# Performance work log

Measured on AMD Instinct MI355X. Metric: run time of the kernel, lower is better.

The kernel has to match this reference:

```python
import jax, jax.numpy as jnp
import numpy as np

B, S, D, H = 4, 2048, 1024, 16
HD = D // H
SCALE = np.sqrt(HD).astype(np.float32)


def setup_inputs() -> dict:
    key = jax.random.key(0)
    ks = jax.random.split(key, 6)
    std = 1.0 / np.sqrt(D)
    return {
        "query": jax.random.normal(ks[0], (B, S, D), jnp.float32),
        "key": jax.random.normal(ks[1], (B, S, D), jnp.float32),
        "value": jax.random.normal(ks[2], (B, S, D), jnp.float32),
        "Wq": jax.random.normal(ks[3], (D, D), jnp.float32) * std,
        "bq": jnp.zeros((D,), jnp.float32),
        "Wk": jax.random.normal(ks[4], (D, D), jnp.float32) * std,
        "bk": jnp.zeros((D,), jnp.float32),
        "Wv": jax.random.normal(ks[5], (D, D), jnp.float32) * std,
        "bv": jnp.zeros((D,), jnp.float32),
    }


def _split_heads(x):
    # [B,S,D] -> [B,H,S,HD]
    return x.reshape(B, S, H, HD).transpose(0, 2, 1, 3)


def reference(query, key, value, Wq, bq, Wk, bk, Wv, bv):
    q = _split_heads(query @ Wq.T + bq)
    k = _split_heads(key @ Wk.T + bk)
    v = _split_heads(value @ Wv.T + bv)
    scores = jnp.einsum("bhqd,bhkd->bhqk", q, k) / SCALE
    attn = jax.nn.softmax(scores, axis=-1)  # dropout=0 (eval)
    ctx = jnp.einsum("bhqk,bhkd->bhqd", attn, v)
    return ctx.transpose(0, 2, 1, 3).reshape(B, S, D)
```

## Files before the change

### kernel.cpp

```cpp
#include <hip/hip_runtime.h>
#include <hip/hip_bf16.h>

typedef __attribute__((ext_vector_type(8))) short bf16x8;
typedef __attribute__((ext_vector_type(4))) float f32x4;
typedef __attribute__((ext_vector_type(16))) float f32x16;

#define SEQ 2048
#define DMODEL 1024
#define NH 16
#define HD 64
#define BATCH 4
#define BHTOT 64
#define BS 8192
#define QKV_ELEMS 8388608

#define C2EXP 0.1803368801111244f

__device__ __forceinline__ ushort f2bf(float f) {
  union { float f; unsigned u; } v; v.f = f;
  unsigned r = (v.u + 0x7FFFu + ((v.u >> 16) & 1u)) >> 16;
  return (ushort)r;
}

__device__ __forceinline__ unsigned pkbf(float a, float b) {
  union { __hip_bfloat162 h; unsigned u; } cv;
  cv.h = __float22bfloat162_rn(make_float2(a, b));
  return cv.u;
}

#if __has_builtin(__builtin_amdgcn_exp2f)
#define EXP2F(x) __builtin_amdgcn_exp2f(x)
#else
#define EXP2F(x) exp2f(x)
#endif

#define GLD16(gp, lp)                                                        \
  __builtin_amdgcn_global_load_lds(                                          \
      (const __attribute__((address_space(1))) void*)(gp),                   \
      (__attribute__((address_space(3))) void*)(lp), 16, 0, 0)

__global__ __launch_bounds__(256) void convert_w(
    const float* __restrict__ w0, const float* __restrict__ w1,
    const float* __restrict__ w2, ushort* __restrict__ out) {
  const float* src = blockIdx.y == 0 ? w0 : (blockIdx.y == 1 ? w1 : w2);
  size_t e = ((size_t)blockIdx.x * 256 + threadIdx.x) * 4;
  float4 v = *(const float4*)(src + e);
  ushort4 o = { f2bf(v.x), f2bf(v.y), f2bf(v.z), f2bf(v.w) };
  *(ushort4*)(out + (size_t)blockIdx.y * 1048576 + e) = o;
}

__global__ __launch_bounds__(256) void convert_x(
    const float* __restrict__ x0, const float* __restrict__ x1,
    const float* __restrict__ x2, ushort* __restrict__ out) {
  const float* src = blockIdx.y == 0 ? x0 : (blockIdx.y == 1 ? x1 : x2);
  size_t e = ((size_t)blockIdx.x * 256 + threadIdx.x) * 4;
  float4 v = *(const float4*)(src + e);
  ushort4 o = { f2bf(v.x), f2bf(v.y), f2bf(v.z), f2bf(v.w) };
  *(ushort4*)(out + (size_t)blockIdx.y * (size_t)QKV_ELEMS + e) = o;
}

__global__ __launch_bounds__(256) void qkv_gemm_bf(
    const ushort* __restrict__ Xb, const ushort* __restrict__ Wb,
    const float* __restrict__ bq, const float* __restrict__ bk, const float* __restrict__ bv,
    ushort* __restrict__ qkv) {
  __shared__ ushort sA[128][32];
  __shared__ ushort sB[128][32];

  const int z = blockIdx.z;
  const ushort* A = Xb + (size_t)z * QKV_ELEMS;
  const ushort* W = Wb + (size_t)z * 1048576;
  const float* bias = z == 0 ? bq : (z == 1 ? bk : bv);
  const float oscale = z == 0 ? C2EXP : 1.0f;
  ushort* out = qkv + (size_t)z * QKV_ELEMS;

  const int t = threadIdx.x;
  const int m0 = blockIdx.x * 128;
  const int n0 = blockIdx.y * 128;
  const int w = t >> 6, l = t & 63, lr = l & 15, lhi = l >> 4;
  const int wr = (w >> 1) * 64, wc = (w & 1) * 64;

  const int rl = l >> 2;
  const int scol = ((l & 3) * 8) ^ ((rl & 3) << 3);
  const int rcol = (lhi * 8) ^ ((lr & 3) << 3);

  f32x4 acc[4][4];
#pragma unroll
  for (int i = 0; i < 4; i++)
#pragma unroll
    for (int j = 0; j < 4; j++) acc[i][j] = (f32x4){0.f, 0.f, 0.f, 0.f};

  for (int k0 = 0; k0 < DMODEL; k0 += 32) {
#pragma unroll
    for (int i = 0; i < 2; i++) {
      int c = w * 2 + i;
      GLD16(A + (size_t)(m0 + c * 16 + rl) * DMODEL + k0 + scol, &sA[c * 16][0]);
      GLD16(W + (size_t)(n0 + c * 16 + rl) * DMODEL + k0 + scol, &sB[c * 16][0]);
    }
    __syncthreads();
    bf16x8 af[4], bfr[4];
#pragma unroll
    for (int mi = 0; mi < 4; mi++) af[mi] = *(const bf16x8*)(&sA[wr + mi * 16 + lr][rcol]);
#pragma unroll
    for (int ni = 0; ni < 4; ni++) bfr[ni] = *(const bf16x8*)(&sB[wc + ni * 16 + lr][rcol]);
#pragma unroll
    for (int mi = 0; mi < 4; mi++)
#pragma unroll
      for (int ni = 0; ni < 4; ni++)
        acc[mi][ni] = __builtin_amdgcn_mfma_f32_16x16x32_bf16(af[mi], bfr[ni], acc[mi][ni], 0, 0, 0);
    __syncthreads();
  }

#pragma unroll
  for (int mi = 0; mi < 4; mi++) {
#pragma unroll
    for (int ni = 0; ni < 4; ni++) {
      int col = n0 + wc + ni * 16 + lr;
      float bsv = bias[col];
      int h = col >> 6, hd = col & 63;
#pragma unroll
      for (int r = 0; r < 4; r++) {
        int row = m0 + wr + mi * 16 + lhi * 4 + r;
        int b = row >> 11, s = row & 2047;
        float vv = (acc[mi][ni][r] + bsv) * oscale;
        out[(((size_t)(b * NH + h)) * SEQ + s) * HD + hd] = f2bf(vv);
      }
    }
  }
}

__global__ __launch_bounds__(256) void qkv_gemm_f32(
    const float* __restrict__ x0, const float* __restrict__ x1, const float* __restrict__ x2,
    const ushort* __restrict__ Wb,
    const float* __restrict__ bq, const float* __restrict__ bk, const float* __restrict__ bv,
    ushort* __restrict__ qkv) {
  __shared__ ushort sA[128][40];
  __shared__ ushort sB[128][40];

  const int z = blockIdx.z;
  const float* X = z == 0 ? x0 : (z == 1 ? x1 : x2);
  const ushort* W = Wb + (size_t)z * 1048576;
  const float* bias = z == 0 ? bq : (z == 1 ? bk : bv);
  const float oscale = z == 0 ? C2EXP : 1.0f;
  ushort* out = qkv + (size_t)z * QKV_ELEMS;

  const int t = threadIdx.x;
  const int m0 = blockIdx.x * 128;
  const int n0 = blockIdx.y * 128;
  const int w = t >> 6, l = t & 63, lr = l & 15, lhi = l >> 4;
  const int wr = (w >> 1) * 64, wc = (w & 1) * 64;

  f32x4 acc[4][4];
#pragma unroll
  for (int i = 0; i < 4; i++)
#pragma unroll
    for (int j = 0; j < 4; j++) acc[i][j] = (f32x4){0.f, 0.f, 0.f, 0.f};

  for (int k0 = 0; k0 < DMODEL; k0 += 32) {
#pragma unroll
    for (int i = 0; i < 4; i++) {
      int e = i * 256 + t;
      int row = e >> 3, col = (e & 7) * 4;
      float4 a = *(const float4*)(X + (size_t)(m0 + row) * DMODEL + k0 + col);
      ushort4 ab = { f2bf(a.x), f2bf(a.y), f2bf(a.z), f2bf(a.w) };
      *(ushort4*)(&sA[row][col]) = ab;
      ushort4 bb = *(const ushort4*)(W + (size_t)(n0 + row) * DMODEL + k0 + col);
      *(ushort4*)(&sB[row][col]) = bb;
    }
    __syncthreads();
    bf16x8 af[4], bfr[4];
#pragma unroll
    for (int mi = 0; mi < 4; mi++) af[mi] = *(const bf16x8*)(&sA[wr + mi * 16 + lr][lhi * 8]);
#pragma unroll
    for (int ni = 0; ni < 4; ni++) bfr[ni] = *(const bf16x8*)(&sB[wc + ni * 16 + lr][lhi * 8]);
#pragma unroll
    for (int mi = 0; mi < 4; mi++)
#pragma unroll
      for (int ni = 0; ni < 4; ni++)
        acc[mi][ni] = __builtin_amdgcn_mfma_f32_16x16x32_bf16(af[mi], bfr[ni], acc[mi][ni], 0, 0, 0);
    __syncthreads();
  }

#pragma unroll
  for (int mi = 0; mi < 4; mi++) {
#pragma unroll
    for (int ni = 0; ni < 4; ni++) {
      int col = n0 + wc + ni * 16 + lr;
      float bsv = bias[col];
      int h = col >> 6, hd = col & 63;
#pragma unroll
      for (int r = 0; r < 4; r++) {
        int row = m0 + wr + mi * 16 + lhi * 4 + r;
        int b = row >> 11, s = row & 2047;
        float vv = (acc[mi][ni][r] + bsv) * oscale;
        out[(((size_t)(b * NH + h)) * SEQ + s) * HD + hd] = f2bf(vv);
      }
    }
  }
}

__global__ __launch_bounds__(256) void transpose_v(const ushort* __restrict__ vsrc,
                                                   ushort* __restrict__ vtg) {
  __shared__ ushort T[64][72];
  const int s0 = blockIdx.x * 64;
  const int bh = blockIdx.y;
  const int t = threadIdx.x;
  const int r = t >> 2, c16 = (t & 3) * 16;

  const ushort* src = vsrc + ((size_t)bh * SEQ + s0 + r) * HD + c16;
  uint4 a = *(const uint4*)(src);
  uint4 b = *(const uint4*)(src + 8);
  *(uint4*)(&T[r][c16]) = a;
  *(uint4*)(&T[r][c16 + 8]) = b;
  __syncthreads();

  ushort o[16];
#pragma unroll
  for (int jj = 0; jj < 16; jj++) {
    int sj = (jj & 3) | ((jj & 4) << 1) | ((jj & 8) >> 1);
    o[jj] = T[c16 + sj][r];
  }
  ushort* dst = vtg + ((size_t)bh * HD + r) * SEQ + s0 + c16;
  *(uint4*)(dst) = *(uint4*)(&o[0]);
  *(uint4*)(dst + 8) = *(uint4*)(&o[8]);
}

__global__ __launch_bounds__(256, 4) void attn_kernel(const ushort* __restrict__ qkv,
                                                      const ushort* __restrict__ vtg,
                                                      float* __restrict__ out) {
  __shared__ ushort Kt[2][64][72];
  __shared__ ushort Vt[2][64][72];

  const int rb = blockIdx.x;
  const int bid = (rb & 7) * 128 + (rb >> 3);
  const int bh = bid >> 4, qt = bid & 15;
  const int q0 = qt * 128;
  const int t = threadIdx.x, w = t >> 6, l = t & 63;
  const int lq = l & 31, hi = l >> 5, hi8 = hi * 8;

  const ushort* q = qkv;
  const size_t base = (size_t)bh * SEQ * HD;
  const ushort* kb = qkv + QKV_ELEMS + base;
  const ushort* vb = vtg + (size_t)bh * HD * SEQ;

  const int rr = t >> 3, kcol = (t & 7) * 8;

  bf16x8 aq[4];
  {
    int qrow = q0 + w * 32 + lq;
#pragma unroll
    for (int ks = 0; ks < 4; ks++)
      aq[ks] = *(const bf16x8*)(q + base + (size_t)qrow * HD + ks * 16 + hi8);
  }

  float m2 = -1e30f, lsum = 0.f;
  f32x16 acc_o[2];
  acc_o[0] = (f32x16)(0.0f);
  acc_o[1] = (f32x16)(0.0f);

#pragma unroll
  for (int i = 0; i < 2; i++) {
    bf16x8 g0 = *(const bf16x8*)(kb + (size_t)(i * 32 + rr) * HD + kcol);
    *(bf16x8*)(&Kt[0][i * 32 + rr][kcol]) = g0;
    bf16x8 g1 = *(const bf16x8*)(vb + (size_t)(i * 32 + rr) * SEQ + kcol);
    *(bf16x8*)(&Vt[0][i * 32 + rr][kcol]) = g1;
  }
  __syncthreads();

  for (int tile = 0; tile < SEQ / 64; tile++) {
    const int cur = tile & 1, nxt = cur ^ 1;
    const int kvn = ((tile + 1) & 31) * 64;

    bf16x8 gk[2], gv[2];
#pragma unroll
    for (int i = 0; i < 2; i++) {
      gk[i] = *(const bf16x8*)(kb + (size_t)(kvn + i * 32 + rr) * HD + kcol);
      gv[i] = *(const bf16x8*)(vb + (size_t)(i * 32 + rr) * SEQ + kvn + kcol);
    }

#pragma unroll
    for (int mt = 0; mt < 2; mt++) {
      f32x16 sc = (f32x16)(0.0f);
#pragma unroll
      for (int ks = 0; ks < 4; ks++) {
        bf16x8 ak = *(const bf16x8*)(&Kt[cur][mt * 32 + lq][ks * 16 + hi8]);
        sc = __builtin_amdgcn_mfma_f32_32x32x16_bf16(ak, aq[ks], sc, 0, 0, 0);
      }

      float tm = fmaxf(sc[0], sc[1]);
#pragma unroll
      for (int r = 2; r < 16; r += 2) tm = fmaxf(fmaxf(sc[r], sc[r + 1]), tm);
      tm = fmaxf(tm, __shfl_xor(tm, 32));
      if (__any(tm > m2 + 8.f)) {
        float mn = fmaxf(m2, tm);
        float alpha = EXP2F(m2 - mn);
        m2 = mn;
        lsum *= alpha;
#pragma unroll
        for (int r = 0; r < 16; r++) {
          int rowq = (r & 3) + 8 * (r >> 2) + 4 * hi;
          float ar = __shfl(alpha, (l & 32) | rowq);
          acc_o[0][r] *= ar;
          acc_o[1][r] *= ar;
        }
      }

      float rs = 0.f;
#pragma unroll
      for (int sp = 0; sp < 2; sp++) {
        const int e0 = sp * 8;
        union { unsigned u[4]; bf16x8 v8; } ap;
#pragma unroll
        for (int j = 0; j < 4; j++) {
          float p0 = EXP2F(sc[e0 + 2 * j] - m2);
          float p1 = EXP2F(sc[e0 + 2 * j + 1] - m2);
          rs += p0 + p1;
          ap.u[j] = pkbf(p0, p1);
        }
        const int s = mt * 2 + sp;
#pragma unroll
        for (int nt = 0; nt < 2; nt++) {
          bf16x8 bv = *(const bf16x8*)(&Vt[cur][nt * 32 + lq][s * 16 + hi8]);
          acc_o[nt] = __builtin_amdgcn_mfma_f32_32x32x16_bf16(ap.v8, bv, acc_o[nt], 0, 0, 0);
        }
      }
      rs += __shfl_xor(rs, 32);
      lsum += rs;
    }

#pragma unroll
    for (int i = 0; i < 2; i++) {
      *(bf16x8*)(&Kt[nxt][i * 32 + rr][kcol]) = gk[i];
      *(bf16x8*)(&Vt[nxt][i * 32 + rr][kcol]) = gv[i];
    }
    __syncthreads();
  }

  const int b = bh >> 4, h = bh & 15;
  float inv = 1.f / lsum;
#pragma unroll
  for (int r = 0; r < 16; r++) {
    int rowq = (r & 3) + 8 * (r >> 2) + 4 * hi;
    float iv = __shfl(inv, (l & 32) | rowq);
    int s = q0 + w * 32 + rowq;
#pragma unroll
    for (int nt = 0; nt < 2; nt++)
      out[((size_t)(b * SEQ + s)) * DMODEL + h * HD + nt * 32 + lq] = acc_o[nt][r] * iv;
  }
}

extern "C" void kernel_launch(void* const* d_in, const int* in_sizes, int n_in,
                              void* d_out, int out_size, void* d_ws, size_t ws_size,
                              hipStream_t stream) {
  const float* query = (const float*)d_in[0];
  const float* key_  = (const float*)d_in[1];
  const float* value = (const float*)d_in[2];
  const float* Wq = (const float*)d_in[3];
  const float* bq = (const float*)d_in[4];
  const float* Wk = (const float*)d_in[5];
  const float* bk = (const float*)d_in[6];
  const float* Wv = (const float*)d_in[7];
  const float* bv = (const float*)d_in[8];

  ushort* Wb = (ushort*)d_ws;
  ushort* qkv = Wb + 3u * 1048576u;
  ushort* Xb = qkv + 3u * (size_t)QKV_ELEMS;
  ushort* Vtg = Xb;
  const size_t need_bf = (3u * 1048576u + 6u * (size_t)QKV_ELEMS) * 2u;
  const size_t need_f32 = (3u * 1048576u + 4u * (size_t)QKV_ELEMS) * 2u;

  convert_w<<<dim3(1024, 3), 256, 0, stream>>>(Wq, Wk, Wv, Wb);
  if (ws_size >= need_bf) {
    convert_x<<<dim3(8192, 3), 256, 0, stream>>>(query, key_, value, Xb);
    qkv_gemm_bf<<<dim3(64, 8, 3), 256, 0, stream>>>(Xb, Wb, bq, bk, bv, qkv);
  } else if (ws_size >= need_f32) {
    qkv_gemm_f32<<<dim3(64, 8, 3), 256, 0, stream>>>(query, key_, value, Wb, bq, bk, bv, qkv);
  }
  transpose_v<<<dim3(SEQ / 64, BHTOT), 256, 0, stream>>>(qkv + 2u * (size_t)QKV_ELEMS, Vtg);
  attn_kernel<<<dim3(BHTOT * (SEQ / 128)), 256, 0, stream>>>(qkv, Vtg, (float*)d_out);
}
```

Measured before the change: 201.3 us.

## Load K fragments directly from global into registers, bypassing LDS

K tiles are no longer staged through shared memory. Each lane now issues inline-asm global_load_dwordx4 for its MFMA K operand one half-tile ahead, waiting with s_waitcnt vmcnt(0) before use. This removes the LDS writes and reads for K and halves LDS usage. V prefetch moves after the first half-tile's PV MFMAs, and the row-sum shuffle is done once per tile. The trade-off is redundant global/L2 traffic, since each of the four waves loads the same K rows. The vmcnt(0) wait also serialises on load latency, and the V loads are now synchronous.

```diff
diff --git a/kernel.cpp b/kernel.cpp
--- a/kernel.cpp
+++ b/kernel.cpp
@@ -39,6 +39,15 @@
       (const __attribute__((address_space(1))) void*)(gp),                   \
       (__attribute__((address_space(3))) void*)(lp), 16, 0, 0)
 
+#define ASYNC_GLB(dst, ptr)                                                  \
+  asm volatile("global_load_dwordx4 %0, %1, off" : "=v"(dst) : "v"(ptr))
+
+#define WAIT_VM0()                                                           \
+  do {                                                                       \
+    asm volatile("s_waitcnt vmcnt(0)" ::: "memory");                         \
+    __builtin_amdgcn_sched_barrier(0);                                       \
+  } while (0)
+
 __global__ __launch_bounds__(256) void convert_w(
     const float* __restrict__ w0, const float* __restrict__ w1,
     const float* __restrict__ w2, ushort* __restrict__ out) {
@@ -227,7 +236,6 @@
 __global__ __launch_bounds__(256, 4) void attn_kernel(const ushort* __restrict__ qkv,
                                                       const ushort* __restrict__ vtg,
                                                       float* __restrict__ out) {
-  __shared__ ushort Kt[2][64][72];
   __shared__ ushort Vt[2][64][72];
 
   const int rb = blockIdx.x;
@@ -243,6 +251,7 @@
   const ushort* vb = vtg + (size_t)bh * HD * SEQ;
 
   const int rr = t >> 3, kcol = (t & 7) * 8;
+  const ushort* kfp = kb + (size_t)lq * HD + hi8;
 
   bf16x8 aq[4];
   {
@@ -257,10 +266,12 @@
   acc_o[0] = (f32x16)(0.0f);
   acc_o[1] = (f32x16)(0.0f);
 
+  bf16x8 kf[4];
+#pragma unroll
+  for (int ks = 0; ks < 4; ks++) ASYNC_GLB(kf[ks], kfp + ks * 16);
+
 #pragma unroll
   for (int i = 0; i < 2; i++) {
-    bf16x8 g0 = *(const bf16x8*)(kb + (size_t)(i * 32 + rr) * HD + kcol);
-    *(bf16x8*)(&Kt[0][i * 32 + rr][kcol]) = g0;
     bf16x8 g1 = *(const bf16x8*)(vb + (size_t)(i * 32 + rr) * SEQ + kcol);
     *(bf16x8*)(&Vt[0][i * 32 + rr][kcol]) = g1;
   }
@@ -268,22 +279,23 @@
 
   for (int tile = 0; tile < SEQ / 64; tile++) {
     const int cur = tile & 1, nxt = cur ^ 1;
+    const int kv0 = tile * 64;
     const int kvn = ((tile + 1) & 31) * 64;
 
-    bf16x8 gk[2], gv[2];
-#pragma unroll
-    for (int i = 0; i < 2; i++) {
-      gk[i] = *(const bf16x8*)(kb + (size_t)(kvn + i * 32 + rr) * HD + kcol);
-      gv[i] = *(const bf16x8*)(vb + (size_t)(i * 32 + rr) * SEQ + kvn + kcol);
-    }
-
+    float rs = 0.f;
 #pragma unroll
     for (int mt = 0; mt < 2; mt++) {
+      WAIT_VM0();
       f32x16 sc = (f32x16)(0.0f);
 #pragma unroll
-      for (int ks = 0; ks < 4; ks++) {
-        bf16x8 ak = *(const bf16x8*)(&Kt[cur][mt * 32 + lq][ks * 16 + hi8]);
-        sc = __builtin_amdgcn_mfma_f32_32x32x16_bf16(ak, aq[ks], sc, 0, 0, 0);
+      for (int ks = 0; ks < 4; ks++)
+        sc = __builtin_amdgcn_mfma_f32_32x32x16_bf16(kf[ks], aq[ks], sc, 0, 0, 0);
+
+      {
+        const size_t knext = (mt == 0) ? (size_t)(kv0 + 32) : (size_t)kvn;
+#pragma unroll
+        for (int ks = 0; ks < 4; ks++)
+          ASYNC_GLB(kf[ks], kfp + knext * HD + ks * 16);
       }
 
       float tm = fmaxf(sc[0], sc[1]);
@@ -304,7 +316,6 @@
         }
       }
 
-      float rs = 0.f;
 #pragma unroll
       for (int sp = 0; sp < 2; sp++) {
         const int e0 = sp * 8;
@@ -323,15 +334,17 @@
           acc_o[nt] = __builtin_amdgcn_mfma_f32_32x32x16_bf16(ap.v8, bv, acc_o[nt], 0, 0, 0);
         }
       }
-      rs += __shfl_xor(rs, 32);
-      lsum += rs;
-    }
-
-#pragma unroll
-    for (int i = 0; i < 2; i++) {
-      *(bf16x8*)(&Kt[nxt][i * 32 + rr][kcol]) = gk[i];
-      *(bf16x8*)(&Vt[nxt][i * 32 + rr][kcol]) = gv[i];
-    }
+
+      if (mt == 0) {
+        bf16x8 gv0 = *(const bf16x8*)(vb + (size_t)rr * SEQ + kvn + kcol);
+        bf16x8 gv1 = *(const bf16x8*)(vb + (size_t)(32 + rr) * SEQ + kvn + kcol);
+        *(bf16x8*)(&Vt[nxt][rr][kcol]) = gv0;
+        *(bf16x8*)(&Vt[nxt][32 + rr][kcol]) = gv1;
+      }
+    }
+
+    rs += __shfl_xor(rs, 32);
+    lsum += rs;
     __syncthreads();
   }
 
```

After: 240.5 us. 19.4% more time.
